# Optimization experiments

Measured on AMD Instinct MI355X. Metric: run time of the kernel, lower is better.

## Reference

```python
import jax, jax.numpy as jnp
import numpy as np

ALPHA = 0.2  # LeakyReLU negative slope
NEG_INF = -9e15


def setup_inputs() -> dict:
    key = jax.random.key(0)
    k1, k2, k3, k4 = jax.random.split(key, 4)
    N, IN_F, OUT_F = 8192, 512, 256
    h = jax.random.normal(k1, (N, IN_F), dtype=jnp.float32)
    adj = jax.random.randint(k2, (N, N), 0, 2).astype(jnp.float32)
    # xavier_uniform for torch Linear weights
    limW = float(np.sqrt(6.0 / (IN_F + OUT_F)))
    W = jax.random.uniform(k3, (OUT_F, IN_F), dtype=jnp.float32, minval=-limW, maxval=limW)
    lima = float(np.sqrt(6.0 / (2 * OUT_F + 1)))
    a_vec = jax.random.uniform(k4, (2 * OUT_F,), dtype=jnp.float32, minval=-lima, maxval=lima)
    return {"h": h, "adj": adj, "W": W, "a_vec": a_vec}


def reference(h, adj, W, a_vec):
    # Wh = W(h), torch Linear: h @ W.T  -> [N, out]
    Wh = h @ W.T
    F_out = W.shape[0]
    # e_ij = leakyrelu(a . [Wh_i, Wh_j]) = leakyrelu(a1.Wh_i + a2.Wh_j)
    s_src = Wh @ a_vec[:F_out]   # [N] contribution of row i
    s_dst = Wh @ a_vec[F_out:]   # [N] contribution of col j
    e = jax.nn.leaky_relu(s_src[:, None] + s_dst[None, :], negative_slope=ALPHA)  # [N, N]
    scores = jnp.where(adj > 0, e, jnp.float32(NEG_INF))
    attention = jax.nn.softmax(scores, axis=1)
    # dropout is identity in eval mode
    h_prime = attention @ Wh  # [N, out]
    return h_prime, attention
```

## Files before the change

### kernel.cpp

```cpp
#include <hip/hip_runtime.h>
#include <stdint.h>

#define N_NODES 8192
#define IN_F    512
#define OUT_F   256
#define ALPHA   0.2f

typedef __attribute__((ext_vector_type(8))) short bf16x8;
typedef __attribute__((ext_vector_type(4))) float f32x4;

__device__ __forceinline__ uint32_t f32_to_bf16(float f) {
    union { float f; uint32_t u; } v; v.f = f;
    uint32_t u = v.u;
    return (u + 0x7fffu + ((u >> 16) & 1u)) >> 16;
}

__device__ __forceinline__ void async_copy16(const void* g, void* l) {
    __builtin_amdgcn_global_load_lds(
        (const __attribute__((address_space(1))) uint32_t*)g,
        (__attribute__((address_space(3))) uint32_t*)l, 16, 0, 0);
}

__global__ __launch_bounds__(256) void k0_wvec(
    const float* __restrict__ W, const float* __restrict__ a_vec,
    float* __restrict__ w12)
{
    const int t  = threadIdx.x;
    const int nb = blockIdx.x * 8;
    float a1lo = 0.f, a1hi = 0.f, a2lo = 0.f, a2hi = 0.f;
    #pragma unroll
    for (int q = 0; q < 8; q++) {
        int n = nb + q;
        float lo = W[(size_t)n * IN_F + t];
        float hi = W[(size_t)n * IN_F + t + 256];
        float a1 = a_vec[n], a2 = a_vec[OUT_F + n];
        a1lo = fmaf(lo, a1, a1lo); a1hi = fmaf(hi, a1, a1hi);
        a2lo = fmaf(lo, a2, a2lo); a2hi = fmaf(hi, a2, a2hi);
    }
    atomicAdd(&w12[t], a1lo);       atomicAdd(&w12[t + 256], a1hi);
    atomicAdd(&w12[512 + t], a2lo); atomicAdd(&w12[512 + t + 256], a2hi);
}

__global__ __launch_bounds__(256) void ks_svec(
    const float* __restrict__ h, const float* __restrict__ w12,
    float* __restrict__ s_src, float* __restrict__ s_dst)
{
    __shared__ float sw[1024];
    const int t = threadIdx.x;
    #pragma unroll
    for (int q = 0; q < 4; q++) sw[q * 256 + t] = w12[q * 256 + t];
    __syncthreads();
    const int w = t >> 6, ln = t & 63;
    const int i = blockIdx.x * 4 + w;
    const float* hr = h + (size_t)i * IN_F + ln * 8;
    float4 h0 = *(const float4*)hr;
    float4 h1 = *(const float4*)(hr + 4);
    const float* w1 = sw + ln * 8;
    const float* w2 = sw + 512 + ln * 8;
    float v1 = h0.x*w1[0] + h0.y*w1[1] + h0.z*w1[2] + h0.w*w1[3]
             + h1.x*w1[4] + h1.y*w1[5] + h1.z*w1[6] + h1.w*w1[7];
    float v2 = h0.x*w2[0] + h0.y*w2[1] + h0.z*w2[2] + h0.w*w2[3]
             + h1.x*w2[4] + h1.y*w2[5] + h1.z*w2[6] + h1.w*w2[7];
    #pragma unroll
    for (int off = 32; off >= 1; off >>= 1) {
        v1 += __shfl_xor(v1, off, 64);
        v2 += __shfl_xor(v2, off, 64);
    }
    if (ln == 0) { s_src[i] = v1; s_dst[i] = v2; }
}

__global__ __launch_bounds__(256) void k1_wh_pack(
    const float* __restrict__ h, const float* __restrict__ W,
    uint16_t* __restrict__ whf)
{
    const int n0 = blockIdx.x * 64, i0 = blockIdx.y * 64;
    const int t  = threadIdx.x;
    const int tn = t & 15, tm = t >> 4;

    __shared__ float As[32][65];
    __shared__ float Bs[32][65];

    float acc[4][4];
    #pragma unroll
    for (int i = 0; i < 4; i++)
        #pragma unroll
        for (int j = 0; j < 4; j++) acc[i][j] = 0.f;

    for (int k0 = 0; k0 < IN_F; k0 += 32) {
        __syncthreads();
        #pragma unroll
        for (int q = 0; q < 2; q++) {
            int u   = q * 256 + t;
            int row = u >> 3;
            int kf  = (u & 7) * 4;
            float4 va = *(const float4*)&h[(size_t)(i0 + row) * IN_F + k0 + kf];
            As[kf + 0][row] = va.x; As[kf + 1][row] = va.y;
            As[kf + 2][row] = va.z; As[kf + 3][row] = va.w;
            float4 vb = *(const float4*)&W[(size_t)(n0 + row) * IN_F + k0 + kf];
            Bs[kf + 0][row] = vb.x; Bs[kf + 1][row] = vb.y;
            Bs[kf + 2][row] = vb.z; Bs[kf + 3][row] = vb.w;
        }
        __syncthreads();
        #pragma unroll
        for (int kk = 0; kk < 32; kk++) {
            float a[4], b[4];
            *(float4*)a = *(const float4*)&As[kk][tm * 4];
            *(float4*)b = *(const float4*)&Bs[kk][tn * 4];
            #pragma unroll
            for (int i = 0; i < 4; i++)
                #pragma unroll
                for (int j = 0; j < 4; j++) acc[i][j] = fmaf(a[i], b[j], acc[i][j]);
        }
    }

    #pragma unroll
    for (int ii = 0; ii < 4; ii++) {
        int gr = i0 + tm * 4 + ii;
        int ck = gr >> 5;
        int lr = (gr >> 3) & 3;
        int jj = gr & 7;
        #pragma unroll
        for (int jn = 0; jn < 4; jn++) {
            int gc   = n0 + tn * 4 + jn;
            int c    = ck * 16 + (gc >> 4);
            int lane = (gc & 15) + lr * 16;
            whf[(size_t)c * 512 + lane * 8 + jj] = (uint16_t)f32_to_bf16(acc[ii][jn]);
        }
    }
}

__global__ __launch_bounds__(256) void k2_mask_l(
    const float* __restrict__ adj, const float* __restrict__ s_src,
    const float* __restrict__ s_dst, uint64_t* __restrict__ mask,
    float* __restrict__ l_out)
{
    const int i = blockIdx.x;
    const int t = threadIdx.x, w = t >> 6, ln = t & 63;
    const float si = s_src[i];
    const float4* rowv = (const float4*)(adj + (size_t)i * N_NODES);
    const float4* sdv  = (const float4*)s_dst;
    float acc = 0.f;
    #pragma unroll 2
    for (int it = 0; it < 8; it++) {
        int jb = it * 4 + w;
        int v4 = jb * 64 + ln;
        float4 a  = rowv[v4];
        float4 sd = sdv[v4];
        uint64_t b0 = __ballot(a.x > 0.f);
        uint64_t b1 = __ballot(a.y > 0.f);
        uint64_t b2 = __ballot(a.z > 0.f);
        uint64_t b3 = __ballot(a.w > 0.f);
        if (ln == 0) {
            uint64_t* mw = mask + (size_t)i * 128 + jb * 4;
            mw[0] = b0; mw[1] = b1; mw[2] = b2; mw[3] = b3;
        }
        float x, e;
        x = si + sd.x; e = fmaxf(x, ALPHA * x); if (a.x > 0.f) acc += __expf(e);
        x = si + sd.y; e = fmaxf(x, ALPHA * x); if (a.y > 0.f) acc += __expf(e);
        x = si + sd.z; e = fmaxf(x, ALPHA * x); if (a.z > 0.f) acc += __expf(e);
        x = si + sd.w; e = fmaxf(x, ALPHA * x); if (a.w > 0.f) acc += __expf(e);
    }
    #pragma unroll
    for (int off = 32; off >= 1; off >>= 1) acc += __shfl_xor(acc, off, 64);
    __shared__ float red[4];
    if (ln == 0) red[w] = acc;
    __syncthreads();
    if (t == 0) l_out[i] = (red[0] + red[1]) + (red[2] + red[3]);
}

__global__ __launch_bounds__(256) void k3_att_gemm(
    const uint64_t* __restrict__ mask, const float* __restrict__ s_src,
    const float* __restrict__ s_dst, const float* __restrict__ l_in,
    const uint16_t* __restrict__ whf, float* __restrict__ att_out,
    float* __restrict__ partial)
{
    const int rb = blockIdx.x, jc = blockIdx.y;
    const int i0 = rb * 32, jbase = jc * 2048;
    const int t = threadIdx.x, w = t >> 6, ln = t & 63;
    const int mh = w & 1, nh = w >> 1;

    __shared__ uint16_t whf_lds[16384];
    __shared__ uint64_t mw[2][32][4];
    __shared__ float    sd[2][64];
    __shared__ float    ssrc[32], invl[32];

    if (t < 32) { ssrc[t] = s_src[i0 + t]; invl[t] = 1.0f / l_in[i0 + t]; }
    if (t < 64) sd[0][t] = s_dst[jbase + t];
    if (t >= 64 && t < 192) {
        int r = (t - 64) >> 2, ph = t & 3;
        mw[0][r][ph] = mask[(size_t)(i0 + r) * 128 + (jbase >> 8) * 4 + ph];
    }

    f32x4 acc[8];
    #pragma unroll
    for (int b = 0; b < 8; b++) acc[b] = (f32x4){0.f, 0.f, 0.f, 0.f};

    const int m   = mh * 16 + (ln & 15);
    const int kof = (ln >> 4) * 8;

    int cur = 0;
    for (int it = 0; it < 32; it++) {
        const int j0 = jbase + it * 64;
        __syncthreads();

        const uint16_t* src = whf + (size_t)(j0 >> 5) * 8192;
        #pragma unroll
        for (int q = 0; q < 8; q++) {
            int c = w * 8 + q;
            async_copy16(src + (size_t)c * 512 + ln * 8, whf_lds + c * 512);
        }

        uint64_t mwv[4];
        #pragma unroll
        for (int ph = 0; ph < 4; ph++) mwv[ph] = mw[cur][m][ph];
        float sim = ssrc[m], il = invl[m];
        int bbase = ((it & 3) << 4) + (kof >> 2);
        float p[2][8];
        #pragma unroll
        for (int ks = 0; ks < 2; ks++) {
            #pragma unroll
            for (int jj = 0; jj < 8; jj++) {
                float x  = sim + sd[cur][ks * 32 + kof + jj];
                float e  = fmaxf(x, ALPHA * x);
                float pe = __expf(e) * il;
                int bidx = bbase + ks * 8 + (jj >> 2);
                p[ks][jj] = ((mwv[jj & 3] >> bidx) & 1ull) ? pe : 0.f;
            }
        }

        if (nh == 0) {
            float* go = att_out + (size_t)(i0 + m) * N_NODES + j0 + kof;
            __builtin_nontemporal_store(*(f32x4*)&p[0][0], (f32x4*)go);
            __builtin_nontemporal_store(*(f32x4*)&p[0][4], (f32x4*)(go + 4));
            __builtin_nontemporal_store(*(f32x4*)&p[1][0], (f32x4*)(go + 32));
            __builtin_nontemporal_store(*(f32x4*)&p[1][4], (f32x4*)(go + 36));
        }

        bf16x8 af[2];
        #pragma unroll
        for (int ks = 0; ks < 2; ks++) {
            union { bf16x8 v; uint32_t u[4]; } pk;
            #pragma unroll
            for (int q = 0; q < 4; q++)
                pk.u[q] = f32_to_bf16(p[ks][2 * q]) | (f32_to_bf16(p[ks][2 * q + 1]) << 16);
            af[ks] = pk.v;
        }

        if (it < 31) {
            int jn = j0 + 64;
            if (t < 64) sd[cur ^ 1][t] = s_dst[jn + t];
            else if (t < 192) {
                int r = (t - 64) >> 2, ph = t & 3;
                mw[cur ^ 1][r][ph] = mask[(size_t)(i0 + r) * 128 + (jn >> 8) * 4 + ph];
            }
        }
        __syncthreads();

        #pragma unroll
        for (int ks = 0; ks < 2; ks++) {
            #pragma unroll
            for (int nl = 0; nl < 8; nl++) {
                int nt = nh * 8 + nl;
                bf16x8 bfr = *(const bf16x8*)(whf_lds + (size_t)(ks * 16 + nt) * 512 + ln * 8);
                acc[nl] = __builtin_amdgcn_mfma_f32_16x16x32_bf16(af[ks], bfr, acc[nl], 0, 0, 0);
            }
        }
        cur ^= 1;
    }

    float* pbase = partial + (size_t)jc * ((size_t)N_NODES * OUT_F);
    int gr0 = i0 + mh * 16 + (ln >> 4) * 4;
    #pragma unroll
    for (int nl = 0; nl < 8; nl++) {
        int gc = nh * 128 + nl * 16 + (ln & 15);
        #pragma unroll
        for (int r = 0; r < 4; r++)
            pbase[(size_t)(gr0 + r) * OUT_F + gc] = acc[nl][r];
    }
}

__global__ __launch_bounds__(256) void k4_reduce(
    const float* __restrict__ partial, float* __restrict__ hp)
{
    const size_t S = (size_t)N_NODES * OUT_F;
    int idx = (blockIdx.x * 256 + threadIdx.x) * 4;
    float4 a = *(const float4*)(partial + idx);
    float4 b = *(const float4*)(partial + S + idx);
    float4 c = *(const float4*)(partial + 2 * S + idx);
    float4 d = *(const float4*)(partial + 3 * S + idx);
    float4 o;
    o.x = (a.x + b.x) + (c.x + d.x);
    o.y = (a.y + b.y) + (c.y + d.y);
    o.z = (a.z + b.z) + (c.z + d.z);
    o.w = (a.w + b.w) + (c.w + d.w);
    *(float4*)(hp + idx) = o;
}

extern "C" void kernel_launch(void* const* d_in, const int* in_sizes, int n_in,
                              void* d_out, int out_size, void* d_ws, size_t ws_size,
                              hipStream_t stream) {
    (void)in_sizes; (void)n_in; (void)out_size; (void)ws_size;
    const float* h     = (const float*)d_in[0];
    const float* adj   = (const float*)d_in[1];
    const float* W     = (const float*)d_in[2];
    const float* a_vec = (const float*)d_in[3];

    char* ws = (char*)d_ws;
    uint16_t* whf  = (uint16_t*)(ws);
    uint64_t* mask = (uint64_t*)(ws + ((size_t)4 << 20));
    float* partial = (float*)(ws + ((size_t)12 << 20));
    float* w12     = (float*)(ws + ((size_t)44 << 20));
    float* s_src   = (float*)(ws + ((size_t)44 << 20) + 16384);
    float* s_dst   = (float*)(ws + ((size_t)44 << 20) + 16384 + 32768);
    float* l_buf   = (float*)(ws + ((size_t)44 << 20) + 16384 + 65536);

    float* hp  = (float*)d_out;
    float* att = hp + (size_t)N_NODES * OUT_F;

    hipMemsetAsync(w12, 0, 4096, stream);
    k0_wvec<<<32, 256, 0, stream>>>(W, a_vec, w12);
    ks_svec<<<2048, 256, 0, stream>>>(h, w12, s_src, s_dst);
    k1_wh_pack<<<dim3(4, 128), 256, 0, stream>>>(h, W, whf);
    k2_mask_l<<<8192, 256, 0, stream>>>(adj, s_src, s_dst, mask, l_buf);
    k3_att_gemm<<<dim3(256, 4), 256, 0, stream>>>(mask, s_src, s_dst, l_buf, whf, att, partial);
    k4_reduce<<<2048, 256, 0, stream>>>(partial, hp);
}
```

Before: 640.4 us.

## Restructure attention GEMM to per-wave rows with direct global B loads

The attention-GEMM kernel now gives each wave its own 16 rows across all 256 output columns, 64 rows per block. B fragments load straight from global memory (via L2) instead of through async LDS staging, and the per-iteration block barriers are gone. This is meant to drop the sync and LDS overhead and stop waves sharing the attention-store work, at the cost of more register pressure (16 accumulators, launch bound of 3 blocks) and repeated global reads of Wh. The Wh pack kernel also stages its bf16 output in LDS so it can write coalesced 16-byte stores, and the adjacency read becomes a nontemporal load.

```diff
diff --git a/kernel.cpp b/kernel.cpp
--- a/kernel.cpp
+++ b/kernel.cpp
@@ -13,12 +13,6 @@
     union { float f; uint32_t u; } v; v.f = f;
     uint32_t u = v.u;
     return (u + 0x7fffu + ((u >> 16) & 1u)) >> 16;
-}
-
-__device__ __forceinline__ void async_copy16(const void* g, void* l) {
-    __builtin_amdgcn_global_load_lds(
-        (const __attribute__((address_space(1))) uint32_t*)g,
-        (__attribute__((address_space(3))) uint32_t*)l, 16, 0, 0);
 }
 
 __global__ __launch_bounds__(256) void k0_wvec(
@@ -79,6 +73,7 @@
 
     __shared__ float As[32][65];
     __shared__ float Bs[32][65];
+    __shared__ uint16_t stg[8192];
 
     float acc[4][4];
     #pragma unroll
@@ -115,17 +110,23 @@
 
     #pragma unroll
     for (int ii = 0; ii < 4; ii++) {
-        int gr = i0 + tm * 4 + ii;
-        int ck = gr >> 5;
-        int lr = (gr >> 3) & 3;
-        int jj = gr & 7;
+        int gr = tm * 4 + ii;
+        int lr = (gr >> 3) & 3, jj = gr & 7, ckl = gr >> 5;
         #pragma unroll
         for (int jn = 0; jn < 4; jn++) {
-            int gc   = n0 + tn * 4 + jn;
-            int c    = ck * 16 + (gc >> 4);
+            int gc = tn * 4 + jn;
+            int lc = ckl * 4 + (gc >> 4);
             int lane = (gc & 15) + lr * 16;
-            whf[(size_t)c * 512 + lane * 8 + jj] = (uint16_t)f32_to_bf16(acc[ii][jn]);
-        }
+            stg[lc * 512 + lane * 8 + jj] = (uint16_t)f32_to_bf16(acc[ii][jn]);
+        }
+    }
+    __syncthreads();
+    {
+        int half = t >> 7, idx = t & 127;
+        int c0 = ((i0 >> 5) + half) * 16 + (n0 >> 4);
+        uint4* g4 = (uint4*)whf + (size_t)c0 * 64 + idx * 2;
+        const uint4* l4 = (const uint4*)stg + half * 256 + idx * 2;
+        g4[0] = l4[0]; g4[1] = l4[1];
     }
 }
 
@@ -137,14 +138,14 @@
     const int i = blockIdx.x;
     const int t = threadIdx.x, w = t >> 6, ln = t & 63;
     const float si = s_src[i];
-    const float4* rowv = (const float4*)(adj + (size_t)i * N_NODES);
-    const float4* sdv  = (const float4*)s_dst;
+    const f32x4* rowv = (const f32x4*)(adj + (size_t)i * N_NODES);
+    const float4* sdv = (const float4*)s_dst;
     float acc = 0.f;
     #pragma unroll 2
     for (int it = 0; it < 8; it++) {
         int jb = it * 4 + w;
         int v4 = jb * 64 + ln;
-        float4 a  = rowv[v4];
+        f32x4 a   = __builtin_nontemporal_load(rowv + v4);
         float4 sd = sdv[v4];
         uint64_t b0 = __ballot(a.x > 0.f);
         uint64_t b1 = __ballot(a.y > 0.f);
@@ -168,114 +169,84 @@
     if (t == 0) l_out[i] = (red[0] + red[1]) + (red[2] + red[3]);
 }
 
-__global__ __launch_bounds__(256) void k3_att_gemm(
+__global__ __launch_bounds__(256, 3) void k3_att_gemm(
     const uint64_t* __restrict__ mask, const float* __restrict__ s_src,
     const float* __restrict__ s_dst, const float* __restrict__ l_in,
     const uint16_t* __restrict__ whf, float* __restrict__ att_out,
     float* __restrict__ partial)
 {
     const int rb = blockIdx.x, jc = blockIdx.y;
-    const int i0 = rb * 32, jbase = jc * 2048;
+    const int i0 = rb * 64, jbase = jc * 2048;
     const int t = threadIdx.x, w = t >> 6, ln = t & 63;
-    const int mh = w & 1, nh = w >> 1;
-
-    __shared__ uint16_t whf_lds[16384];
-    __shared__ uint64_t mw[2][32][4];
-    __shared__ float    sd[2][64];
-    __shared__ float    ssrc[32], invl[32];
-
-    if (t < 32) { ssrc[t] = s_src[i0 + t]; invl[t] = 1.0f / l_in[i0 + t]; }
-    if (t < 64) sd[0][t] = s_dst[jbase + t];
-    if (t >= 64 && t < 192) {
-        int r = (t - 64) >> 2, ph = t & 3;
-        mw[0][r][ph] = mask[(size_t)(i0 + r) * 128 + (jbase >> 8) * 4 + ph];
-    }
-
-    f32x4 acc[8];
-    #pragma unroll
-    for (int b = 0; b < 8; b++) acc[b] = (f32x4){0.f, 0.f, 0.f, 0.f};
-
-    const int m   = mh * 16 + (ln & 15);
+    const int m   = ln & 15;
     const int kof = (ln >> 4) * 8;
 
-    int cur = 0;
+    const int row = i0 + w * 16 + m;
+    const float sim = s_src[row];
+    const float il  = 1.0f / l_in[row];
+    const uint64_t* mrow = mask + (size_t)row * 128 + jc * 32;
+    float* arow = att_out + (size_t)row * N_NODES;
+
+    f32x4 acc[16];
+    #pragma unroll
+    for (int b = 0; b < 16; b++) acc[b] = (f32x4){0.f, 0.f, 0.f, 0.f};
+
+    uint64_t mwv[4];
     for (int it = 0; it < 32; it++) {
-        const int j0 = jbase + it * 64;
-        __syncthreads();
-
-        const uint16_t* src = whf + (size_t)(j0 >> 5) * 8192;
-        #pragma unroll
-        for (int q = 0; q < 8; q++) {
-            int c = w * 8 + q;
-            async_copy16(src + (size_t)c * 512 + ln * 8, whf_lds + c * 512);
-        }
-
-        uint64_t mwv[4];
-        #pragma unroll
-        for (int ph = 0; ph < 4; ph++) mwv[ph] = mw[cur][m][ph];
-        float sim = ssrc[m], il = invl[m];
-        int bbase = ((it & 3) << 4) + (kof >> 2);
+        const int J0 = jbase + it * 64;
+        if ((it & 3) == 0) {
+            const ulonglong2* mp = (const ulonglong2*)(mrow + (it >> 2) * 4);
+            ulonglong2 m01 = mp[0], m23 = mp[1];
+            mwv[0] = m01.x; mwv[1] = m01.y; mwv[2] = m23.x; mwv[3] = m23.y;
+        }
         float p[2][8];
         #pragma unroll
         for (int ks = 0; ks < 2; ks++) {
+            float4 s0 = *(const float4*)(s_dst + J0 + ks * 32 + kof);
+            float4 s1 = *(const float4*)(s_dst + J0 + ks * 32 + kof + 4);
+            float sdv[8] = {s0.x, s0.y, s0.z, s0.w, s1.x, s1.y, s1.z, s1.w};
+            int bb = ((it & 3) << 4) + (ks << 3) + (kof >> 2);
             #pragma unroll
             for (int jj = 0; jj < 8; jj++) {
-                float x  = sim + sd[cur][ks * 32 + kof + jj];
+                float x  = sim + sdv[jj];
                 float e  = fmaxf(x, ALPHA * x);
                 float pe = __expf(e) * il;
-                int bidx = bbase + ks * 8 + (jj >> 2);
-                p[ks][jj] = ((mwv[jj & 3] >> bidx) & 1ull) ? pe : 0.f;
+                p[ks][jj] = ((mwv[jj & 3] >> (bb + (jj >> 2))) & 1ull) ? pe : 0.f;
             }
         }
-
-        if (nh == 0) {
-            float* go = att_out + (size_t)(i0 + m) * N_NODES + j0 + kof;
+        {
+            float* go = arow + J0 + kof;
             __builtin_nontemporal_store(*(f32x4*)&p[0][0], (f32x4*)go);
             __builtin_nontemporal_store(*(f32x4*)&p[0][4], (f32x4*)(go + 4));
             __builtin_nontemporal_store(*(f32x4*)&p[1][0], (f32x4*)(go + 32));
             __builtin_nontemporal_store(*(f32x4*)&p[1][4], (f32x4*)(go + 36));
         }
-
-        bf16x8 af[2];
         #pragma unroll
         for (int ks = 0; ks < 2; ks++) {
             union { bf16x8 v; uint32_t u[4]; } pk;
             #pragma unroll
             for (int q = 0; q < 4; q++)
                 pk.u[q] = f32_to_bf16(p[ks][2 * q]) | (f32_to_bf16(p[ks][2 * q + 1]) << 16);
-            af[ks] = pk.v;
-        }
-
-        if (it < 31) {
-            int jn = j0 + 64;
-            if (t < 64) sd[cur ^ 1][t] = s_dst[jn + t];
-            else if (t < 192) {
-                int r = (t - 64) >> 2, ph = t & 3;
-                mw[cur ^ 1][r][ph] = mask[(size_t)(i0 + r) * 128 + (jn >> 8) * 4 + ph];
+            bf16x8 af = pk.v;
+            const uint4* bsrc = (const uint4*)whf
+                + ((size_t)((jbase + it * 64) >> 5) + ks) * 1024 + ln;
+            #pragma unroll
+            for (int nt = 0; nt < 16; nt++) {
+                bf16x8 bfr;
+                *(uint4*)&bfr = bsrc[nt * 64];
+                acc[nt] = __builtin_amdgcn_mfma_f32_16x16x32_bf16(af, bfr, acc[nt], 0, 0, 0);
             }
         }
-        __syncthreads();
-
-        #pragma unroll
-        for (int ks = 0; ks < 2; ks++) {
-            #pragma unroll
-            for (int nl = 0; nl < 8; nl++) {
-                int nt = nh * 8 + nl;
-                bf16x8 bfr = *(const bf16x8*)(whf_lds + (size_t)(ks * 16 + nt) * 512 + ln * 8);
-                acc[nl] = __builtin_amdgcn_mfma_f32_16x16x32_bf16(af[ks], bfr, acc[nl], 0, 0, 0);
-            }
-        }
-        cur ^= 1;
     }
 
     float* pbase = partial + (size_t)jc * ((size_t)N_NODES * OUT_F);
-    int gr0 = i0 + mh * 16 + (ln >> 4) * 4;
-    #pragma unroll
-    for (int nl = 0; nl < 8; nl++) {
-        int gc = nh * 128 + nl * 16 + (ln & 15);
+    int gr0 = i0 + w * 16 + (ln >> 4) * 4;
+    #pragma unroll
+    for (int nt = 0; nt < 16; nt++) {
+        int gc = nt * 16 + m;
         #pragma unroll
         for (int r = 0; r < 4; r++)
-            pbase[(size_t)(gr0 + r) * OUT_F + gc] = acc[nl][r];
+            pbase[(size_t)(gr0 + r) * OUT_F + gc] = acc[nt][r];
     }
 }
 
@@ -317,11 +288,11 @@
     float* hp  = (float*)d_out;
     float* att = hp + (size_t)N_NODES * OUT_F;
 
-    hipMemsetAsync(w12, 0, 4096, stream);
+    (void)hipMemsetAsync(w12, 0, 4096, stream);
     k0_wvec<<<32, 256, 0, stream>>>(W, a_vec, w12);
     ks_svec<<<2048, 256, 0, stream>>>(h, w12, s_src, s_dst);
     k1_wh_pack<<<dim3(4, 128), 256, 0, stream>>>(h, W, whf);
     k2_mask_l<<<8192, 256, 0, stream>>>(adj, s_src, s_dst, mask, l_buf);
-    k3_att_gemm<<<dim3(256, 4), 256, 0, stream>>>(mask, s_src, s_dst, l_buf, whf, att, partial);
+    k3_att_gemm<<<dim3(128, 4), 256, 0, stream>>>(mask, s_src, s_dst, l_buf, whf, att, partial);
     k4_reduce<<<2048, 256, 0, stream>>>(partial, hp);
 }
```

Result: slower. 777.3 us (+21.4%).
